# Kernel tuning notes

Measured on AMD Instinct MI355X. Metric: run time of the kernel, lower is better.

The kernel has to match this reference:

```python
import jax, jax.numpy as jnp
import numpy as np

N, NFEAT, NHID, NCLASS, NHEAD = 8192, 512, 64, 16, 4
ALPHA = 0.1  # leaky relu slope
NEG = -9e15


def setup_inputs() -> dict:
    key = jax.random.key(0)
    ks = jax.random.split(key, 7)
    x = jax.random.normal(ks[0], (N, NFEAT), dtype=jnp.float32)
    adj = (jax.random.uniform(ks[1], (N, N)) < 0.05).astype(jnp.float32)
    # per-head params: W [H, nfeat, nhid], a [H, 2*nhid] (xavier-ish scale)
    W = jax.random.normal(ks[2], (NHEAD, NFEAT, NHID), dtype=jnp.float32) * (1.0 / np.sqrt(NFEAT))
    a = jax.random.normal(ks[3], (NHEAD, 2 * NHID), dtype=jnp.float32) * (1.0 / np.sqrt(NHID))
    W_out = jax.random.normal(ks[4], (NHEAD * NHID, NCLASS), dtype=jnp.float32) * (1.0 / np.sqrt(NHEAD * NHID))
    a_out = jax.random.normal(ks[5], (2 * NCLASS,), dtype=jnp.float32) * (1.0 / np.sqrt(NCLASS))
    return {"x": x, "adj": adj, "W": W, "a": a, "W_out": W_out, "a_out": a_out}


def _gat_layer(h, adj, Wk, ak):
    """Dense pyGAT GraphAttentionLayer (eval mode, dropout = identity)."""
    d = Wk.shape[1]
    Wh = h @ Wk                         # [N, d]
    f1 = Wh @ ak[:d]                    # [N]
    f2 = Wh @ ak[d:]                    # [N]
    e = jax.nn.leaky_relu(f1[:, None] + f2[None, :], negative_slope=ALPHA)  # [N, N]
    att = jax.nn.softmax(jnp.where(adj > 0, e, NEG), axis=1)
    return att @ Wh                     # [N, d]


def reference(x, adj, W, a, W_out, a_out):
    # eval mode: F.dropout is identity
    heads = jax.vmap(lambda Wk, ak: jax.nn.elu(_gat_layer(x, adj, Wk, ak)))(W, a)  # [H, N, nhid]
    h = jnp.transpose(heads, (1, 0, 2)).reshape(x.shape[0], -1)                    # [N, H*nhid]
    out = jax.nn.elu(_gat_layer(h, adj, W_out, a_out))                             # [N, nclass]
    return jax.nn.log_softmax(out, axis=1)
```

## Files before the change

### kernel.cpp

```cpp
#include <hip/hip_runtime.h>
#include <hip/hip_bf16.h>

#define NN 8192
#define NFEAT 512
#define NHID 64
#define NCLASS 16
#define NHEAD 4
#define ALPHA 0.1f
#define ZSPLIT 4
#define JPB (NN / ZSPLIT)
#define DCH 128
#define Z2 8
#define JPB2 (NN / Z2)

typedef short bf16x8 __attribute__((ext_vector_type(8)));
typedef float f32x4 __attribute__((ext_vector_type(4)));
typedef float fv4 __attribute__((ext_vector_type(4)));

__device__ __forceinline__ float lrelu(float x) { return fmaxf(x, ALPHA * x); }
__device__ __forceinline__ float elu(float x) { return x > 0.f ? x : __expf(x) - 1.f; }
__device__ __forceinline__ short f2b(float x) {
  union { __bf16 b; short s; } c; c.b = (__bf16)x; return c.s;
}
__device__ __forceinline__ float b2f(short x) {
  union { unsigned int u; float f; } c; c.u = ((unsigned int)(unsigned short)x) << 16; return c.f;
}

__global__ __launch_bounds__(256) void k_wprep(const float* __restrict__ W,
                                               short* __restrict__ WB) {
  __shared__ float t[64][65];
  const int h = blockIdx.y;
  const int k0 = blockIdx.x * 64;
  const int tid = threadIdx.x;
#pragma unroll
  for (int it = 0; it < 16; ++it) {
    const int r = it * 4 + (tid >> 6), c = tid & 63;
    t[r][c] = W[((size_t)h * NFEAT + k0 + r) * NHID + c];
  }
  __syncthreads();
#pragma unroll
  for (int it = 0; it < 16; ++it) {
    const int d = it * 4 + (tid >> 6), k = tid & 63;
    WB[((size_t)h * NHID + d) * NFEAT + k0 + k] = f2b(t[k][d]);
  }
}

__global__ __launch_bounds__(256) void k_prep1(const float* __restrict__ x,
                                               const short* __restrict__ WB,
                                               const float* __restrict__ a,
                                               short* __restrict__ Whf,
                                               float* __restrict__ f1i,
                                               float* __restrict__ f2i) {
  __shared__ short tile[64][72];
  const int bid = blockIdx.x;
  const int h = bid >> 7;
  const int bm = (bid & 127) * 64;
  const int tid = threadIdx.x;
  const int wv = tid >> 6, lane = tid & 63;
  const int mr = lane & 15, kg = lane >> 4;
  f32x4 acc0 = {0.f, 0.f, 0.f, 0.f}, acc1 = acc0, acc2 = acc0, acc3 = acc0;
  const float* ap = x + (size_t)(bm + wv * 16 + mr) * NFEAT + kg * 8;
  const short* bp = WB + ((size_t)h * NHID + mr) * NFEAT + kg * 8;
#pragma unroll 2
  for (int k0 = 0; k0 < NFEAT; k0 += 32) {
    const float4 xa = *reinterpret_cast<const float4*>(ap);
    const float4 xb = *reinterpret_cast<const float4*>(ap + 4);
    bf16x8 af;
    af[0] = f2b(xa.x); af[1] = f2b(xa.y); af[2] = f2b(xa.z); af[3] = f2b(xa.w);
    af[4] = f2b(xb.x); af[5] = f2b(xb.y); af[6] = f2b(xb.z); af[7] = f2b(xb.w);
    const bf16x8 b0 = *reinterpret_cast<const bf16x8*>(bp);
    const bf16x8 b1 = *reinterpret_cast<const bf16x8*>(bp + 16 * NFEAT);
    const bf16x8 b2 = *reinterpret_cast<const bf16x8*>(bp + 32 * NFEAT);
    const bf16x8 b3 = *reinterpret_cast<const bf16x8*>(bp + 48 * NFEAT);
    acc0 = __builtin_amdgcn_mfma_f32_16x16x32_bf16(af, b0, acc0, 0, 0, 0);
    acc1 = __builtin_amdgcn_mfma_f32_16x16x32_bf16(af, b1, acc1, 0, 0, 0);
    acc2 = __builtin_amdgcn_mfma_f32_16x16x32_bf16(af, b2, acc2, 0, 0, 0);
    acc3 = __builtin_amdgcn_mfma_f32_16x16x32_bf16(af, b3, acc3, 0, 0, 0);
    ap += 32; bp += 32;
  }
  float a1v[4], a2v[4];
#pragma unroll
  for (int c = 0; c < 4; ++c) {
    a1v[c] = a[h * 128 + mr + c * 16];
    a2v[c] = a[h * 128 + 64 + mr + c * 16];
  }
#pragma unroll
  for (int q = 0; q < 4; ++q) {
    float s1 = acc0[q] * a1v[0] + acc1[q] * a1v[1] + acc2[q] * a1v[2] + acc3[q] * a1v[3];
    float s2 = acc0[q] * a2v[0] + acc1[q] * a2v[1] + acc2[q] * a2v[2] + acc3[q] * a2v[3];
#pragma unroll
    for (int off = 1; off < 16; off <<= 1) {
      s1 += __shfl_xor(s1, off);
      s2 += __shfl_xor(s2, off);
    }
    if (mr == 0) {
      const int i = bm + wv * 16 + kg * 4 + q;
      f1i[(size_t)i * 4 + h] = s1;
      f2i[(size_t)i * 4 + h] = s2;
    }
  }
#pragma unroll
  for (int q = 0; q < 4; ++q) {
    const int r = wv * 16 + kg * 4 + q;
    tile[r][mr +  0] = f2b(acc0[q]);
    tile[r][mr + 16] = f2b(acc1[q]);
    tile[r][mr + 32] = f2b(acc2[q]);
    tile[r][mr + 48] = f2b(acc3[q]);
  }
  __syncthreads();
#pragma unroll
  for (int it = 0; it < 2; ++it) {
    const int jbl = (tid >> 6) + it * 4;
    const int d = tid & 63;
    bf16x8 o;
#pragma unroll
    for (int jo = 0; jo < 8; ++jo) o[jo] = tile[jbl * 8 + jo][d];
    *reinterpret_cast<bf16x8*>(Whf +
        (((size_t)h * 1024 + (bm >> 3) + jbl) * 64 + d) * 8) = o;
  }
}

__global__ __launch_bounds__(256) void k_rmax(const float* __restrict__ src,
                                              float* __restrict__ dst, int n, int stride,
                                              int boff) {
  const float* p = src + (size_t)blockIdx.x * boff;
  float m = -1e30f;
  for (int k = threadIdx.x; k < n; k += 256) m = fmaxf(m, p[(size_t)k * stride]);
#pragma unroll
  for (int off = 32; off; off >>= 1) m = fmaxf(m, __shfl_xor(m, off));
  __shared__ float sm[4];
  if ((threadIdx.x & 63) == 0) sm[threadIdx.x >> 6] = m;
  __syncthreads();
  if (threadIdx.x == 0) dst[blockIdx.x] = fmaxf(fmaxf(sm[0], sm[1]), fmaxf(sm[2], sm[3]));
}

__global__ __launch_bounds__(256) void k_acbd(const float* __restrict__ f1i,
                                              const float* __restrict__ f2i,
                                              const float* __restrict__ f2max,
                                              float2* __restrict__ ACh,
                                              unsigned int* __restrict__ BDh) {
  const int idx = blockIdx.x * 256 + threadIdx.x;
  const int i = idx & (NN - 1);
  const int h = idx >> 13;
  const float fm = f2max[h];
  const float f1 = f1i[(size_t)i * 4 + h];
  const float f2 = f2i[(size_t)i * 4 + h];
  const float s = f1 + fm;
  const float mrow = fmaxf(s, 0.1f * s);
  float2 ac;
  ac.x = __expf(s - mrow);
  ac.y = __expf(0.1f * s - mrow);
  ACh[(size_t)h * NN + i] = ac;
  const float t = f2 - fm;
  const unsigned int B = (unsigned short)f2b(__expf(t));
  const unsigned int D = (unsigned short)f2b(__expf(0.1f * t));
  BDh[(size_t)h * NN + i] = B | (D << 16);
}

__global__ __launch_bounds__(256) void k_acbd2(const float* __restrict__ f1o,
                                               const float* __restrict__ f2o,
                                               const float* __restrict__ f2omax,
                                               float2* __restrict__ AC2,
                                               unsigned int* __restrict__ BD2) {
  const int i = blockIdx.x * 256 + threadIdx.x;
  const float fm = f2omax[0];
  const float f1 = f1o[i];
  const float f2 = f2o[i];
  const float s = f1 + fm;
  const float mrow = fmaxf(s, 0.1f * s);
  float2 ac;
  ac.x = __expf(s - mrow);
  ac.y = __expf(0.1f * s - mrow);
  AC2[i] = ac;
  const float t = f2 - fm;
  const unsigned int B = (unsigned short)f2b(__expf(t));
  const unsigned int D = (unsigned short)f2b(__expf(0.1f * t));
  BD2[i] = B | (D << 16);
}

__global__ __launch_bounds__(256) void k_scan(const float* __restrict__ adj,
                                              unsigned int* __restrict__ bmask) {
  const fv4* a4 = reinterpret_cast<const fv4*>(adj);
  const int t0 = blockIdx.x * 256 + threadIdx.x;
#pragma unroll 4
  for (int it = 0; it < 32; ++it) {
    const int g = it * 524288 + t0;
    const fv4 v = __builtin_nontemporal_load(a4 + g);
    unsigned int nv = (unsigned int)((v.x > 0.f) | ((v.y > 0.f) << 1) |
                                     ((v.z > 0.f) << 2) | ((v.w > 0.f) << 3))
                      << ((threadIdx.x & 7) * 4);
    nv |= __shfl_xor(nv, 1);
    nv |= __shfl_xor(nv, 2);
    nv |= __shfl_xor(nv, 4);
    if ((threadIdx.x & 7) == 0) bmask[g >> 3] = nv;
  }
}

__global__ __launch_bounds__(256) void k_dense1z(const unsigned int* __restrict__ bmask,
                                                 const short* __restrict__ Whf,
                                                 const float2* __restrict__ ACh,
                                                 const unsigned int* __restrict__ BDh,
                                                 float* __restrict__ OpP,
                                                 float* __restrict__ rsP) {
  __shared__ short sm_b[16 * 64 * 8];
  __shared__ unsigned int sm_bd[DCH];
  __shared__ unsigned int sm_mask[64][5];
  const int i0 = blockIdx.x * 64;
  const int h = blockIdx.y;
  const int z = blockIdx.z;
  const int jb0 = z * JPB;
  const int tid = threadIdx.x;
  const int wv = tid >> 6, lane = tid & 63;
  const int mr = lane & 15, kg = lane >> 4;
  const int row_local = wv * 16 + mr;
  const float2 ac = ACh[(size_t)h * NN + i0 + row_local];
  f32x4 acc0 = {0.f, 0.f, 0.f, 0.f}, acc1 = acc0, acc2 = acc0, acc3 = acc0;
  float rs = 0.f;

  for (int jc = jb0; jc < jb0 + JPB; jc += DCH) {
    __syncthreads();
    {
      sm_mask[tid >> 2][tid & 3] =
          bmask[(size_t)(i0 + (tid >> 2)) * 256 + (jc >> 5) + (tid & 3)];
      if (tid < DCH) sm_bd[tid] = BDh[(size_t)h * NN + jc + tid];
      const uint4* src = reinterpret_cast<const uint4*>(
          Whf + ((size_t)h * 1024 + (jc >> 3)) * 512);
      uint4* dst = reinterpret_cast<uint4*>(sm_b);
#pragma unroll
      for (int u = 0; u < 4; ++u) dst[tid + u * 256] = src[tid + u * 256];
    }
    __syncthreads();
#pragma unroll
    for (int ks = 0; ks < DCH / 32; ++ks) {
      const int jl = ks * 32 + kg * 8;
      const uint4 bda = *reinterpret_cast<const uint4*>(&sm_bd[jl]);
      const uint4 bdb = *reinterpret_cast<const uint4*>(&sm_bd[jl + 4]);
      const unsigned int mb = (sm_mask[row_local][(jc - jb0) / 32 % 4 == 0 ? ks : ks]
                               >> 0);
      (void)mb;
      const unsigned int mbb = (sm_mask[row_local][ks] >> (kg * 8)) & 0xffu;
      bf16x8 af;
#define MKW(e, bdw)                                              \
      {                                                          \
        const float Bf = __uint_as_float((bdw) << 16);           \
        const float Df = __uint_as_float((bdw) & 0xffff0000u);   \
        float w_ = fmaxf(ac.x * Bf, ac.y * Df);                  \
        w_ = ((mbb >> (e)) & 1u) ? w_ : 0.f;                     \
        rs += w_;                                                \
        af[e] = f2b(w_);                                         \
      }
      MKW(0, bda.x) MKW(1, bda.y) MKW(2, bda.z) MKW(3, bda.w)
      MKW(4, bdb.x) MKW(5, bdb.y) MKW(6, bdb.z) MKW(7, bdb.w)
#undef MKW
      const short* wp = sm_b + ((size_t)(jl >> 3) * 64 + mr) * 8;
      const bf16x8 bf0 = *reinterpret_cast<const bf16x8*>(wp);
      const bf16x8 bf1 = *reinterpret_cast<const bf16x8*>(wp + 128);
      const bf16x8 bf2 = *reinterpret_cast<const bf16x8*>(wp + 256);
      const bf16x8 bf3 = *reinterpret_cast<const bf16x8*>(wp + 384);
      acc0 = __builtin_amdgcn_mfma_f32_16x16x32_bf16(af, bf0, acc0, 0, 0, 0);
      acc1 = __builtin_amdgcn_mfma_f32_16x16x32_bf16(af, bf1, acc1, 0, 0, 0);
      acc2 = __builtin_amdgcn_mfma_f32_16x16x32_bf16(af, bf2, acc2, 0, 0, 0);
      acc3 = __builtin_amdgcn_mfma_f32_16x16x32_bf16(af, bf3, acc3, 0, 0, 0);
    }
  }
  rs += __shfl_xor(rs, 16);
  rs += __shfl_xor(rs, 32);
  if (lane < 16)
    rsP[((size_t)z * NHEAD + h) * NN + i0 + wv * 16 + lane] = rs;
  float* op = OpP + (((size_t)z * NHEAD + h) * NN + i0) * 64;
#pragma unroll
  for (int q = 0; q < 4; ++q) {
    const int r = wv * 16 + kg * 4 + q;
    op[(size_t)r * 64 + mr +  0] = acc0[q];
    op[(size_t)r * 64 + mr + 16] = acc1[q];
    op[(size_t)r * 64 + mr + 32] = acc2[q];
    op[(size_t)r * 64 + mr + 48] = acc3[q];
  }
}

__global__ __launch_bounds__(256) void k_comb1(const float* __restrict__ OpP,
                                               const float* __restrict__ rsP,
                                               short* __restrict__ hcat) {
  const int idx = blockIdx.x * 256 + threadIdx.x;
  const int i = idx >> 8;
  const int hc = idx & 255;
  const int h = hc >> 6, d = hc & 63;
  float s = 0.f, rsum = 0.f;
#pragma unroll
  for (int z = 0; z < ZSPLIT; ++z) {
    s += OpP[(((size_t)z * NHEAD + h) * NN + i) * 64 + d];
    rsum += rsP[((size_t)z * NHEAD + h) * NN + i];
  }
  hcat[idx] = f2b(elu(s / rsum));
}

__global__ __launch_bounds__(256) void k_gemm2(const short* __restrict__ hcat,
                                               const float* __restrict__ Wout,
                                               const float* __restrict__ aout,
                                               short* __restrict__ Wh2f,
                                               float* __restrict__ f1o,
                                               float* __restrict__ f2o) {
  __shared__ float sW[NHEAD * NHID][NCLASS + 1];
  __shared__ float sh[16][NHEAD * NHID + 1];
  const int tid = threadIdx.x;
  const int r = tid >> 4, c = tid & 15;
  const int row = blockIdx.x * 16 + r;
  for (int u = tid; u < 256 * 16; u += 256) sW[u >> 4][u & 15] = Wout[u];
  for (int u = tid; u < 16 * 256; u += 256)
    sh[u >> 8][u & 255] = b2f(hcat[(size_t)(blockIdx.x * 16 + (u >> 8)) * 256 + (u & 255)]);
  __syncthreads();
  float acc = 0.f;
#pragma unroll 8
  for (int f = 0; f < 256; ++f) acc += sh[r][f] * sW[f][c];
  Wh2f[(((size_t)blockIdx.x * 2 + (r >> 3)) * 16 + c) * 8 + (r & 7)] = f2b(acc);
  float s1 = acc * aout[c];
  float s2 = acc * aout[NCLASS + c];
#pragma unroll
  for (int off = 8; off; off >>= 1) { s1 += __shfl_xor(s1, off); s2 += __shfl_xor(s2, off); }
  if (c == 0) { f1o[row] = s1; f2o[row] = s2; }
}

__global__ __launch_bounds__(256) void k_dense2z(const unsigned int* __restrict__ bmask,
                                                 const short* __restrict__ Wh2f,
                                                 const float2* __restrict__ AC2,
                                                 const unsigned int* __restrict__ BD2,
                                                 float* __restrict__ Op2P,
                                                 float* __restrict__ rs2P) {
  __shared__ unsigned int sm_mask[64][33];
  const int i0 = blockIdx.x * 64;
  const int z = blockIdx.y;
  const int jb0 = z * JPB2;
  const int tid = threadIdx.x;
  {
    const int row = tid >> 2;
    const int w0 = (tid & 3) * 8;
#pragma unroll
    for (int u = 0; u < 8; ++u)
      sm_mask[row][w0 + u] = bmask[(size_t)(i0 + row) * 256 + (jb0 >> 5) + w0 + u];
  }
  __syncthreads();
  const int wv = tid >> 6, lane = tid & 63;
  const int mr = lane & 15, kg = lane >> 4;
  const int row_local = wv * 16 + mr;
  const float2 ac = AC2[i0 + row_local];
  f32x4 acc = {0.f, 0.f, 0.f, 0.f};
  float rs = 0.f;
  const unsigned int* bd = BD2 + jb0;
  const short* w2 = Wh2f + (size_t)(jb0 >> 3) * 128 + mr * 8;
#pragma unroll 2
  for (int ks = 0; ks < 32; ++ks) {
    const int jl = ks * 32 + kg * 8;
    const uint4 bda = *reinterpret_cast<const uint4*>(bd + jl);
    const uint4 bdb = *reinterpret_cast<const uint4*>(bd + jl + 4);
    const unsigned int mbb = (sm_mask[row_local][ks] >> (kg * 8)) & 0xffu;
    bf16x8 af;
#define MKW(e, bdw)                                              \
    {                                                            \
      const float Bf = __uint_as_float((bdw) << 16);             \
      const float Df = __uint_as_float((bdw) & 0xffff0000u);     \
      float w_ = fmaxf(ac.x * Bf, ac.y * Df);                    \
      w_ = ((mbb >> (e)) & 1u) ? w_ : 0.f;                       \
      rs += w_;                                                  \
      af[e] = f2b(w_);                                           \
    }
    MKW(0, bda.x) MKW(1, bda.y) MKW(2, bda.z) MKW(3, bda.w)
    MKW(4, bdb.x) MKW(5, bdb.y) MKW(6, bdb.z) MKW(7, bdb.w)
#undef MKW
    const bf16x8 bf = *reinterpret_cast<const bf16x8*>(w2 + (size_t)(jl >> 3) * 128);
    acc = __builtin_amdgcn_mfma_f32_16x16x32_bf16(af, bf, acc, 0, 0, 0);
  }
  rs += __shfl_xor(rs, 16);
  rs += __shfl_xor(rs, 32);
  if (lane < 16)
    rs2P[(size_t)z * NN + i0 + wv * 16 + lane] = rs;
  float* op = Op2P + ((size_t)z * NN + i0) * NCLASS;
#pragma unroll
  for (int q = 0; q < 4; ++q)
    op[(size_t)(wv * 16 + kg * 4 + q) * NCLASS + mr] = acc[q];
}

__global__ __launch_bounds__(256) void k_comb2(const float* __restrict__ Op2P,
                                               const float* __restrict__ rs2P,
                                               float* __restrict__ out) {
  const int idx = blockIdx.x * 256 + threadIdx.x;
  const int i = idx >> 4;
  const int c = idx & 15;
  float s = 0.f, rsum = 0.f;
#pragma unroll
  for (int z = 0; z < Z2; ++z) {
    s += Op2P[((size_t)z * NN + i) * NCLASS + c];
    rsum += rs2P[(size_t)z * NN + i];
  }
  const float v = elu(s / rsum);
  float vm = v;
#pragma unroll
  for (int off = 8; off; off >>= 1) vm = fmaxf(vm, __shfl_xor(vm, off, 16));
  float ex = __expf(v - vm);
#pragma unroll
  for (int off = 8; off; off >>= 1) ex += __shfl_xor(ex, off, 16);
  out[idx] = v - vm - __logf(ex);
}

extern "C" void kernel_launch(void* const* d_in, const int* in_sizes, int n_in,
                              void* d_out, int out_size, void* d_ws, size_t ws_size,
                              hipStream_t stream) {
  const float* x    = (const float*)d_in[0];
  const float* adj  = (const float*)d_in[1];
  const float* W    = (const float*)d_in[2];
  const float* a    = (const float*)d_in[3];
  const float* Wout = (const float*)d_in[4];
  const float* aout = (const float*)d_in[5];
  float* out = (float*)d_out;
  char* ws = (char*)d_ws;
  const size_t MB = 1048576;
  const size_t KB = 1024;

  unsigned int* bmask  = (unsigned int*)(ws);
  short* Whf           = (short*)(ws + 8 * MB);
  short* hcat          = (short*)(ws + 12 * MB);
  float* OpP           = (float*)(ws + 16 * MB);
  float* rsP           = (float*)(ws + 48 * MB);
  float* Op2P          = (float*)(ws + 49 * MB);
  float* rs2P          = (float*)(ws + 53 * MB);
  short* WB            = (short*)(ws + 54 * MB);
  float* f1i           = (float*)(ws + 54 * MB + 256 * KB);
  float* f2i           = (float*)(ws + 54 * MB + 384 * KB);
  float2* ACh          = (float2*)(ws + 54 * MB + 512 * KB);
  unsigned int* BDh    = (unsigned int*)(ws + 54 * MB + 768 * KB);
  float* f1o           = (float*)(ws + 54 * MB + 896 * KB);
  float* f2o           = (float*)(ws + 54 * MB + 928 * KB);
  short* Wh2f          = (short*)(ws + 54 * MB + 960 * KB);
  float2* AC2          = (float2*)(ws + 54 * MB + 1216 * KB);
  unsigned int* BD2    = (unsigned int*)(ws + 54 * MB + 1280 * KB);
  float* f2max         = (float*)(ws + 54 * MB + 1312 * KB);
  float* f2omax        = (float*)(ws + 54 * MB + 1312 * KB + 64);

  k_wprep<<<dim3(8, 4), 256, 0, stream>>>(W, WB);
  k_prep1<<<512, 256, 0, stream>>>(x, WB, a, Whf, f1i, f2i);
  k_rmax<<<NHEAD, 256, 0, stream>>>(f2i, f2max, NN, 4, 1);
  k_acbd<<<NN * NHEAD / 256, 256, 0, stream>>>(f1i, f2i, f2max, ACh, BDh);
  k_scan<<<2048, 256, 0, stream>>>(adj, bmask);
  k_dense1z<<<dim3(NN / 64, NHEAD, ZSPLIT), 256, 0, stream>>>(bmask, Whf, ACh, BDh, OpP, rsP);
  k_comb1<<<NN, 256, 0, stream>>>(OpP, rsP, hcat);
  k_gemm2<<<NN / 16, 256, 0, stream>>>(hcat, Wout, aout, Wh2f, f1o, f2o);
  k_rmax<<<1, 256, 0, stream>>>(f2o, f2omax, NN, 1, 0);
  k_acbd2<<<NN / 256, 256, 0, stream>>>(f1o, f2o, f2omax, AC2, BD2);
  k_dense2z<<<dim3(NN / 64, Z2), 256, 0, stream>>>(bmask, Wh2f, AC2, BD2, Op2P, rs2P);
  k_comb2<<<NN * NCLASS / 256, 256, 0, stream>>>(Op2P, rs2P, out);
}
```

Before: 216.0 us.

## Fuse column-max into producer kernels via atomics and prefetch dense1 tiles

Removes the two standalone k_rmax launches. The producer kernels now compute per-block maxima of f2 and combine them with atomicMax on an order-preserving unsigned key, after a memset clears the keys. In k_dense1z, the next chunk's mask, BD and Wh tile are loaded into registers while the current chunk is being computed, which should hide global-memory latency. The costs are one extra memset launch, atomics, and higher register pressure in the dense kernel.

```diff
diff --git a/kernel.cpp b/kernel.cpp
--- a/kernel.cpp
+++ b/kernel.cpp
@@ -25,6 +25,14 @@
 __device__ __forceinline__ float b2f(short x) {
   union { unsigned int u; float f; } c; c.u = ((unsigned int)(unsigned short)x) << 16; return c.f;
 }
+__device__ __forceinline__ unsigned int fkey(float f) {
+  const unsigned int b = __float_as_uint(f);
+  return (b & 0x80000000u) ? ~b : (b | 0x80000000u);
+}
+__device__ __forceinline__ float funkey(unsigned int k) {
+  const unsigned int b = (k & 0x80000000u) ? (k & 0x7fffffffu) : ~k;
+  return __uint_as_float(b);
+}
 
 __global__ __launch_bounds__(256) void k_wprep(const float* __restrict__ W,
                                                short* __restrict__ WB) {
@@ -50,8 +58,10 @@
                                                const float* __restrict__ a,
                                                short* __restrict__ Whf,
                                                float* __restrict__ f1i,
-                                               float* __restrict__ f2i) {
+                                               float* __restrict__ f2i,
+                                               unsigned int* __restrict__ f2maxK) {
   __shared__ short tile[64][72];
+  __shared__ float bmx[4];
   const int bid = blockIdx.x;
   const int h = bid >> 7;
   const int bm = (bid & 127) * 64;
@@ -84,6 +94,7 @@
     a1v[c] = a[h * 128 + mr + c * 16];
     a2v[c] = a[h * 128 + 64 + mr + c * 16];
   }
+  float m2 = -1e30f;
 #pragma unroll
   for (int q = 0; q < 4; ++q) {
     float s1 = acc0[q] * a1v[0] + acc1[q] * a1v[1] + acc2[q] * a1v[2] + acc3[q] * a1v[3];
@@ -93,12 +104,16 @@
       s1 += __shfl_xor(s1, off);
       s2 += __shfl_xor(s2, off);
     }
+    m2 = fmaxf(m2, s2);
     if (mr == 0) {
       const int i = bm + wv * 16 + kg * 4 + q;
       f1i[(size_t)i * 4 + h] = s1;
       f2i[(size_t)i * 4 + h] = s2;
     }
   }
+  m2 = fmaxf(m2, __shfl_xor(m2, 16));
+  m2 = fmaxf(m2, __shfl_xor(m2, 32));
+  if (lane == 0) bmx[wv] = m2;
 #pragma unroll
   for (int q = 0; q < 4; ++q) {
     const int r = wv * 16 + kg * 4 + q;
@@ -108,6 +123,8 @@
     tile[r][mr + 48] = f2b(acc3[q]);
   }
   __syncthreads();
+  if (tid == 0)
+    atomicMax(f2maxK + h, fkey(fmaxf(fmaxf(bmx[0], bmx[1]), fmaxf(bmx[2], bmx[3]))));
 #pragma unroll
   for (int it = 0; it < 2; ++it) {
     const int jbl = (tid >> 6) + it * 4;
@@ -120,29 +137,15 @@
   }
 }
 
-__global__ __launch_bounds__(256) void k_rmax(const float* __restrict__ src,
-                                              float* __restrict__ dst, int n, int stride,
-                                              int boff) {
-  const float* p = src + (size_t)blockIdx.x * boff;
-  float m = -1e30f;
-  for (int k = threadIdx.x; k < n; k += 256) m = fmaxf(m, p[(size_t)k * stride]);
-#pragma unroll
-  for (int off = 32; off; off >>= 1) m = fmaxf(m, __shfl_xor(m, off));
-  __shared__ float sm[4];
-  if ((threadIdx.x & 63) == 0) sm[threadIdx.x >> 6] = m;
-  __syncthreads();
-  if (threadIdx.x == 0) dst[blockIdx.x] = fmaxf(fmaxf(sm[0], sm[1]), fmaxf(sm[2], sm[3]));
-}
-
 __global__ __launch_bounds__(256) void k_acbd(const float* __restrict__ f1i,
                                               const float* __restrict__ f2i,
-                                              const float* __restrict__ f2max,
+                                              const unsigned int* __restrict__ f2maxK,
                                               float2* __restrict__ ACh,
                                               unsigned int* __restrict__ BDh) {
   const int idx = blockIdx.x * 256 + threadIdx.x;
   const int i = idx & (NN - 1);
   const int h = idx >> 13;
-  const float fm = f2max[h];
+  const float fm = funkey(f2maxK[h]);
   const float f1 = f1i[(size_t)i * 4 + h];
   const float f2 = f2i[(size_t)i * 4 + h];
   const float s = f1 + fm;
@@ -159,11 +162,11 @@
 
 __global__ __launch_bounds__(256) void k_acbd2(const float* __restrict__ f1o,
                                                const float* __restrict__ f2o,
-                                               const float* __restrict__ f2omax,
+                                               const unsigned int* __restrict__ f2omaxK,
                                                float2* __restrict__ AC2,
                                                unsigned int* __restrict__ BD2) {
   const int i = blockIdx.x * 256 + threadIdx.x;
-  const float fm = f2omax[0];
+  const float fm = funkey(f2omaxK[0]);
   const float f1 = f1o[i];
   const float f2 = f2o[i];
   const float s = f1 + fm;
@@ -216,28 +219,37 @@
   const float2 ac = ACh[(size_t)h * NN + i0 + row_local];
   f32x4 acc0 = {0.f, 0.f, 0.f, 0.f}, acc1 = acc0, acc2 = acc0, acc3 = acc0;
   float rs = 0.f;
-
-  for (int jc = jb0; jc < jb0 + JPB; jc += DCH) {
+  const int NCH = JPB / DCH;
+
+  unsigned int rM, rBD;
+  uint4 rB0, rB1, rB2, rB3;
+#define LOADR(jc)                                                              \
+  {                                                                            \
+    rM = bmask[(size_t)(i0 + (tid >> 2)) * 256 + ((jc) >> 5) + (tid & 3)];     \
+    rBD = BDh[(size_t)h * NN + (jc) + (tid & (DCH - 1))];                      \
+    const uint4* src_ = reinterpret_cast<const uint4*>(                       \
+        Whf + ((size_t)h * 1024 + ((jc) >> 3)) * 512);                         \
+    rB0 = src_[tid];                                                           \
+    rB1 = src_[tid + 256];                                                     \
+    rB2 = src_[tid + 512];                                                     \
+    rB3 = src_[tid + 768];                                                     \
+  }
+  LOADR(jb0)
+  for (int c = 0; c < NCH; ++c) {
     __syncthreads();
+    sm_mask[tid >> 2][tid & 3] = rM;
+    if (tid < DCH) sm_bd[tid] = rBD;
     {
-      sm_mask[tid >> 2][tid & 3] =
-          bmask[(size_t)(i0 + (tid >> 2)) * 256 + (jc >> 5) + (tid & 3)];
-      if (tid < DCH) sm_bd[tid] = BDh[(size_t)h * NN + jc + tid];
-      const uint4* src = reinterpret_cast<const uint4*>(
-          Whf + ((size_t)h * 1024 + (jc >> 3)) * 512);
       uint4* dst = reinterpret_cast<uint4*>(sm_b);
-#pragma unroll
-      for (int u = 0; u < 4; ++u) dst[tid + u * 256] = src[tid + u * 256];
+      dst[tid] = rB0; dst[tid + 256] = rB1; dst[tid + 512] = rB2; dst[tid + 768] = rB3;
     }
+    if (c + 1 < NCH) LOADR(jb0 + (c + 1) * DCH)
     __syncthreads();
 #pragma unroll
     for (int ks = 0; ks < DCH / 32; ++ks) {
       const int jl = ks * 32 + kg * 8;
       const uint4 bda = *reinterpret_cast<const uint4*>(&sm_bd[jl]);
       const uint4 bdb = *reinterpret_cast<const uint4*>(&sm_bd[jl + 4]);
-      const unsigned int mb = (sm_mask[row_local][(jc - jb0) / 32 % 4 == 0 ? ks : ks]
-                               >> 0);
-      (void)mb;
       const unsigned int mbb = (sm_mask[row_local][ks] >> (kg * 8)) & 0xffu;
       bf16x8 af;
 #define MKW(e, bdw)                                              \
@@ -263,6 +275,7 @@
       acc3 = __builtin_amdgcn_mfma_f32_16x16x32_bf16(af, bf3, acc3, 0, 0, 0);
     }
   }
+#undef LOADR
   rs += __shfl_xor(rs, 16);
   rs += __shfl_xor(rs, 32);
   if (lane < 16)
@@ -299,9 +312,11 @@
                                                const float* __restrict__ aout,
                                                short* __restrict__ Wh2f,
                                                float* __restrict__ f1o,
-                                               float* __restrict__ f2o) {
+                                               float* __restrict__ f2o,
+                                               unsigned int* __restrict__ f2omaxK) {
   __shared__ float sW[NHEAD * NHID][NCLASS + 1];
   __shared__ float sh[16][NHEAD * NHID + 1];
+  __shared__ float bmx[4];
   const int tid = threadIdx.x;
   const int r = tid >> 4, c = tid & 15;
   const int row = blockIdx.x * 16 + r;
@@ -318,6 +333,13 @@
 #pragma unroll
   for (int off = 8; off; off >>= 1) { s1 += __shfl_xor(s1, off); s2 += __shfl_xor(s2, off); }
   if (c == 0) { f1o[row] = s1; f2o[row] = s2; }
+  float m2 = s2;
+  m2 = fmaxf(m2, __shfl_xor(m2, 16));
+  m2 = fmaxf(m2, __shfl_xor(m2, 32));
+  if ((tid & 63) == 0) bmx[tid >> 6] = m2;
+  __syncthreads();
+  if (tid == 0)
+    atomicMax(f2omaxK, fkey(fmaxf(fmaxf(bmx[0], bmx[1]), fmaxf(bmx[2], bmx[3]))));
 }
 
 __global__ __launch_bounds__(256) void k_dense2z(const unsigned int* __restrict__ bmask,
@@ -432,19 +454,18 @@
   short* Wh2f          = (short*)(ws + 54 * MB + 960 * KB);
   float2* AC2          = (float2*)(ws + 54 * MB + 1216 * KB);
   unsigned int* BD2    = (unsigned int*)(ws + 54 * MB + 1280 * KB);
-  float* f2max         = (float*)(ws + 54 * MB + 1312 * KB);
-  float* f2omax        = (float*)(ws + 54 * MB + 1312 * KB + 64);
-
+  unsigned int* f2maxK = (unsigned int*)(ws + 54 * MB + 1312 * KB);
+  unsigned int* f2omaxK = f2maxK + 4;
+
+  hipMemsetAsync(f2maxK, 0, 8 * sizeof(unsigned int), stream);
   k_wprep<<<dim3(8, 4), 256, 0, stream>>>(W, WB);
-  k_prep1<<<512, 256, 0, stream>>>(x, WB, a, Whf, f1i, f2i);
-  k_rmax<<<NHEAD, 256, 0, stream>>>(f2i, f2max, NN, 4, 1);
-  k_acbd<<<NN * NHEAD / 256, 256, 0, stream>>>(f1i, f2i, f2max, ACh, BDh);
+  k_prep1<<<512, 256, 0, stream>>>(x, WB, a, Whf, f1i, f2i, f2maxK);
+  k_acbd<<<NN * NHEAD / 256, 256, 0, stream>>>(f1i, f2i, f2maxK, ACh, BDh);
   k_scan<<<2048, 256, 0, stream>>>(adj, bmask);
   k_dense1z<<<dim3(NN / 64, NHEAD, ZSPLIT), 256, 0, stream>>>(bmask, Whf, ACh, BDh, OpP, rsP);
   k_comb1<<<NN, 256, 0, stream>>>(OpP, rsP, hcat);
-  k_gemm2<<<NN / 16, 256, 0, stream>>>(hcat, Wout, aout, Wh2f, f1o, f2o);
-  k_rmax<<<1, 256, 0, stream>>>(f2o, f2omax, NN, 1, 0);
-  k_acbd2<<<NN / 256, 256, 0, stream>>>(f1o, f2o, f2omax, AC2, BD2);
+  k_gemm2<<<NN / 16, 256, 0, stream>>>(hcat, Wout, aout, Wh2f, f1o, f2o, f2omaxK);
+  k_acbd2<<<NN / 256, 256, 0, stream>>>(f1o, f2o, f2omaxK, AC2, BD2);
   k_dense2z<<<dim3(NN / 64, Z2), 256, 0, stream>>>(bmask, Wh2f, AC2, BD2, Op2P, rs2P);
   k_comb2<<<NN * NCLASS / 256, 256, 0, stream>>>(Op2P, rs2P, out);
 }
```

Measured after the change: 212.6 us (median of 2 runs). About the same (-1.6%).
